# Kernel tuning notes

Measured on AMD Instinct MI355X. Metric: run time of the kernel, lower is better.

## Reference

```python
import jax, jax.numpy as jnp
import numpy as np

L = 6          # layers in stage
B = 8          # batch
NH = 16        # heads
F = 1024       # features per token
FH = F // NH   # features per head (64)
GH, GW = 24, 24
N = 1 + GH * GW  # 577 tokens (readout + patches)
HID = 4 * F


def _relpos_index():
    # BEiT-style relative position index over the (1+H*W) token grid
    coords = np.stack(np.meshgrid(np.arange(GH), np.arange(GW), indexing='ij')).reshape(2, -1)
    rel = (coords[:, :, None] - coords[:, None, :]).transpose(1, 2, 0).astype(np.int64)
    rel[..., 0] += GH - 1
    rel[..., 1] += GW - 1
    rel[..., 0] *= 2 * GW - 1
    nrd = (2 * GH - 1) * (2 * GW - 1) + 3  # num relative distances (+3 for readout token)
    idx = np.zeros((N, N), np.int64)
    idx[1:, 1:] = rel.sum(-1)
    idx[0, :] = nrd - 3
    idx[:, 0] = nrd - 2
    idx[0, 0] = nrd - 1
    return idx, nrd

REL_IDX_NP, NRD = _relpos_index()
REL_IDX = jnp.asarray(REL_IDX_NP)


def _ln(x, g, b):
    m = x.mean(-1, keepdims=True)
    v = ((x - m) ** 2).mean(-1, keepdims=True)
    return (x - m) / jnp.sqrt(v + 1e-6) * g + b


def setup_inputs() -> dict:
    key = jax.random.key(0)
    ks = jax.random.split(key, 16)
    s = 0.02
    return {
        'tokens': jax.random.normal(ks[0], (B, N, F), jnp.float32),
        'ln1_g': jnp.ones((L, F), jnp.float32),
        'ln1_b': jnp.zeros((L, F), jnp.float32),
        'q_bias': jax.random.normal(ks[1], (L, 1, NH, 1, FH), jnp.float32) * s,
        'v_bias': jax.random.normal(ks[2], (L, 1, NH, 1, FH), jnp.float32) * s,
        'qkv_w': jax.random.normal(ks[3], (L, 3 * F, F), jnp.float32) * s,
        'relpos_table': jax.random.normal(ks[4], (L, NRD, NH), jnp.float32) * s,
        'proj_w': jax.random.normal(ks[5], (L, F, F), jnp.float32) * s,
        'proj_b': jnp.zeros((L, F), jnp.float32),
        'scale_attn': jnp.full((L, F), 0.1, jnp.float32),
        'ln2_g': jnp.ones((L, F), jnp.float32),
        'ln2_b': jnp.zeros((L, F), jnp.float32),
        'mlp_w1': jax.random.normal(ks[6], (L, HID, F), jnp.float32) * s,
        'mlp_b1': jnp.zeros((L, HID), jnp.float32),
        'mlp_w2': jax.random.normal(ks[7], (L, F, HID), jnp.float32) * s,
        'mlp_b2': jnp.zeros((L, F), jnp.float32),
        'scale_mlp': jnp.full((L, F), 0.1, jnp.float32),
    }


def reference(tokens, ln1_g, ln1_b, q_bias, v_bias, qkv_w, relpos_table, proj_w, proj_b,
              scale_attn, ln2_g, ln2_b, mlp_w1, mlp_b1, mlp_w2, mlp_b2, scale_mlp):
    qk_scale = FH ** (-0.5)
    x = tokens
    for i in range(L):
        # --- attention branch ---
        h = _ln(x, ln1_g[i], ln1_b[i])                       # [B,N,F]
        qkv = (h @ qkv_w[i].T).reshape(B, N, 3, NH, FH)
        qkv = qkv.transpose(2, 0, 3, 1, 4)                   # [3,B,H,N,f]
        q = (qkv[0] + q_bias[i]) * qk_scale
        k = qkv[1]
        v = qkv[2] + v_bias[i]
        attn = jnp.einsum('bhnf,bhmf->bhnm', q, k)           # [B,H,N,N]
        bias = relpos_table[i][REL_IDX].transpose(2, 0, 1)   # [H,N,N]
        w = jax.nn.softmax(attn + bias[None], axis=-1)
        out = jnp.einsum('bhnm,bhmf->bhnf', w, v)
        out = out.transpose(0, 2, 1, 3).reshape(B, N, F)
        out = out @ proj_w[i].T + proj_b[i]
        x = x + scale_attn[i] * out
        # --- MLP branch ---
        h2 = _ln(x, ln2_g[i], ln2_b[i])
        m = jax.nn.gelu(h2 @ mlp_w1[i].T + mlp_b1[i], approximate=False)
        m = m @ mlp_w2[i].T + mlp_b2[i]
        x = x + scale_mlp[i] * m
    return x
```

## Files before the change

### kernel.cpp

```cpp
#include <hip/hip_runtime.h>
#include <cstdint>
#include <cstddef>

typedef __bf16 bf16;
typedef __bf16 bf16x8 __attribute__((ext_vector_type(8)));
typedef __bf16 bf16x4v __attribute__((ext_vector_type(4)));
typedef float f32x4 __attribute__((ext_vector_type(4)));
typedef unsigned int u32x4 __attribute__((ext_vector_type(4)));

static constexpr int NB = 8, NH = 16, F = 1024, FH = 64, NTOK = 577, NPAD = 640;
static constexpr int NLAYER = 6, HID = 4096, NRD = 2212;
static constexpr int MROWS = NB * NPAD;

static constexpr size_t H_OFF    = 0;
static constexpr size_t Q_OFF    = H_OFF    + (size_t)MROWS*F*2;
static constexpr size_t K_OFF    = Q_OFF    + (size_t)NB*NH*NPAD*FH*2;
static constexpr size_t V_OFF    = K_OFF    + (size_t)NB*NH*NPAD*FH*2;
static constexpr size_t O_OFF    = V_OFF    + (size_t)NB*NH*FH*NPAD*2;
static constexpr size_t BIAS_OFF = O_OFF    + (size_t)MROWS*F*2;
static constexpr size_t M1_OFF   = BIAS_OFF + (size_t)NH*NPAD*NPAD*4;
static constexpr size_t WQKV_OFF = M1_OFF   + (size_t)MROWS*HID*2;
static constexpr size_t WPROJ_OFF= WQKV_OFF + (size_t)3*F*F*2;
static constexpr size_t WM1_OFF  = WPROJ_OFF+ (size_t)F*F*2;
static constexpr size_t WM2_OFF  = WM1_OFF  + (size_t)HID*F*2;
static constexpr size_t WS_NEED  = WM2_OFF  + (size_t)HID*F*2;

__device__ __forceinline__ f32x4 mfma16(bf16x8 a, bf16x8 b, f32x4 c) {
  return __builtin_amdgcn_mfma_f32_16x16x32_bf16(a, b, c, 0, 0, 0);
}

__device__ __forceinline__ void gload16(const bf16* g, bf16* l) {
  __builtin_amdgcn_global_load_lds(
      (const __attribute__((address_space(1))) void*)g,
      (__attribute__((address_space(3))) void*)l, 16, 0, 0);
}

__global__ __launch_bounds__(256) void copy_kernel(const float* __restrict__ s, float* __restrict__ d) {
  size_t i = ((size_t)blockIdx.x*256 + threadIdx.x)*4;
  *(float4*)(d + i) = *(const float4*)(s + i);
}

static constexpr int CVT_N0 = 3*F*F;
static constexpr int CVT_N1 = CVT_N0 + F*F;
static constexpr int CVT_N2 = CVT_N1 + HID*F;
static constexpr int CVT_N3 = CVT_N2 + F*HID;
__global__ __launch_bounds__(256) void cvt4_kernel(
    const float* __restrict__ s0, const float* __restrict__ s1,
    const float* __restrict__ s2, const float* __restrict__ s3,
    bf16* __restrict__ d0, bf16* __restrict__ d1,
    bf16* __restrict__ d2, bf16* __restrict__ d3) {
  int i = (blockIdx.x*256 + threadIdx.x)*4;
  const float* s; bf16* d; int off;
  if (i < CVT_N0)      { s = s0; d = d0; off = i; }
  else if (i < CVT_N1) { s = s1; d = d1; off = i - CVT_N0; }
  else if (i < CVT_N2) { s = s2; d = d2; off = i - CVT_N1; }
  else                 { s = s3; d = d3; off = i - CVT_N2; }
  float4 v = *(const float4*)(s + off);
  bf16x4v o;
  o[0] = (bf16)v.x; o[1] = (bf16)v.y; o[2] = (bf16)v.z; o[3] = (bf16)v.w;
  *(bf16x4v*)(d + off) = o;
}

__global__ __launch_bounds__(256) void ln_kernel(const float* __restrict__ X,
    const float* __restrict__ g, const float* __restrict__ bta, bf16* __restrict__ H) {
  int row = blockIdx.x;
  int bb = row / NTOK, tok = row % NTOK;
  const float* x = X + (size_t)row * F;
  int tid = threadIdx.x;
  float4 v = *(const float4*)(x + tid*4);
  float s  = v.x + v.y + v.z + v.w;
  float s2 = v.x*v.x + v.y*v.y + v.z*v.z + v.w*v.w;
  #pragma unroll
  for (int off = 1; off < 64; off <<= 1) {
    s  += __shfl_xor(s,  off, 64);
    s2 += __shfl_xor(s2, off, 64);
  }
  __shared__ float red[8];
  int w = tid >> 6;
  if ((tid & 63) == 0) { red[w] = s; red[4+w] = s2; }
  __syncthreads();
  s  = red[0]+red[1]+red[2]+red[3];
  s2 = red[4]+red[5]+red[6]+red[7];
  float mean = s * (1.0f/1024.0f);
  float var  = s2 * (1.0f/1024.0f) - mean*mean;
  float rstd = rsqrtf(fmaxf(var, 0.0f) + 1e-6f);
  float4 gg  = *(const float4*)(g + tid*4);
  float4 bb4 = *(const float4*)(bta + tid*4);
  bf16x4v o;
  o[0] = (bf16)((v.x-mean)*rstd*gg.x + bb4.x);
  o[1] = (bf16)((v.y-mean)*rstd*gg.y + bb4.y);
  o[2] = (bf16)((v.z-mean)*rstd*gg.z + bb4.z);
  o[3] = (bf16)((v.w-mean)*rstd*gg.w + bb4.w);
  *(bf16x4v*)(H + ((size_t)bb*NPAD + tok)*F + tid*4) = o;
}

__global__ __launch_bounds__(256) void bias_kernel(const float* __restrict__ table, float* __restrict__ bias) {
  int bi = blockIdx.x;
  int h = bi / NPAD, n = bi % NPAD;
  float* out = bias + ((size_t)h*NPAD + n)*NPAD;
  for (int m = threadIdx.x; m < NPAD; m += 256) {
    float val;
    if (n >= NTOK || m >= NTOK) val = -1e30f;
    else {
      int idx;
      if (n == 0 && m == 0) idx = NRD - 1;
      else if (m == 0)      idx = NRD - 2;
      else if (n == 0)      idx = NRD - 3;
      else {
        int pn = n - 1, pm = m - 1;
        int rn = pn / 24, cn = pn % 24, rm = pm / 24, cm = pm % 24;
        idx = (rn - rm + 23)*47 + (cn - cm + 23);
      }
      val = table[idx*NH + h];
    }
    out[m] = val;
  }
}

template<int BMT, int EPI>
__global__ __launch_bounds__(256, 2)
void gemm_kernel(const bf16* __restrict__ A, const bf16* __restrict__ Bw, int K, int ldc,
                 const float* __restrict__ p0, const float* __restrict__ p1,
                 float* __restrict__ xout, bf16* __restrict__ bout,
                 bf16* __restrict__ q_out, bf16* __restrict__ k_out, bf16* __restrict__ v_out)
{
  constexpr int BM = 64*BMT;
  constexpr int WN = (BMT==2) ? 2 : 4;
  constexpr int NF = 128/(WN*16);
  __shared__ bf16 As[BM*32], Bs[128*32];
  const int tid = threadIdx.x;
  const int lane = tid & 63, w = tid >> 6;
  const int wm = (BMT==2) ? (w>>1) : 0;
  const int wn = (BMT==2) ? (w&1) : w;
  const int lg = lane >> 4, lr = lane & 15;
  const int m0 = blockIdx.x * BM, n0 = blockIdx.y * 128;

  const f32x4 fz = {0.f, 0.f, 0.f, 0.f};
  f32x4 acc[4][NF];
  #pragma unroll
  for (int i = 0; i < 4; ++i)
    #pragma unroll
    for (int j = 0; j < NF; ++j) acc[i][j] = fz;

  const int srow = lane >> 2;
  const int scol = (lane & 3) * 8;

  const int klen = K / (int)gridDim.z;
  const int kbeg = (int)blockIdx.z * klen;

  for (int kt = kbeg; kt < kbeg + klen; kt += 32) {
    if (BMT == 2) {
      #pragma unroll
      for (int j = 0; j < 2; ++j) {
        int li = w + j*4;
        gload16(A + (size_t)(m0 + li*16 + srow)*K + kt + scol, &As[li*512]);
      }
    } else {
      gload16(A + (size_t)(m0 + w*16 + srow)*K + kt + scol, &As[w*512]);
    }
    #pragma unroll
    for (int j = 0; j < 2; ++j) {
      int li = w*2 + j;
      gload16(Bw + (size_t)(n0 + li*16 + srow)*K + kt + scol, &Bs[li*512]);
    }
    __syncthreads();
    bf16x8 af[4], bfv[NF];
    #pragma unroll
    for (int f = 0; f < 4; ++f)
      af[f]  = *(const bf16x8*)&As[(wm*64 + f*16 + lr)*32 + lg*8];
    #pragma unroll
    for (int f = 0; f < NF; ++f)
      bfv[f] = *(const bf16x8*)&Bs[(wn*(NF*16) + f*16 + lr)*32 + lg*8];
    #pragma unroll
    for (int mf = 0; mf < 4; ++mf)
      #pragma unroll
      for (int nf = 0; nf < NF; ++nf)
        acc[mf][nf] = mfma16(af[mf], bfv[nf], acc[mf][nf]);
    __syncthreads();
  }

  #pragma unroll
  for (int mf = 0; mf < 4; ++mf) {
    const int row = m0 + wm*64 + mf*16 + lg*4;
    const int bidx = row / NPAD;
    const int tokbase = row - bidx*NPAD;
    #pragma unroll
    for (int nf = 0; nf < NF; ++nf) {
      const int col = n0 + wn*(NF*16) + nf*16 + lr;
      if (EPI == 0) {
        const int sec = col >> 10, ci = col & 1023;
        const int hh = ci >> 6, fh = ci & 63;
        const size_t bhh = (size_t)bidx*NH + hh;
        #pragma unroll
        for (int r = 0; r < 4; ++r) {
          float v = acc[mf][nf][r];
          if (sec == 0)      q_out[(bhh*NPAD + tokbase + r)*FH + fh] = (bf16)((v + p0[ci]) * 0.125f);
          else if (sec == 1) k_out[(bhh*NPAD + tokbase + r)*FH + fh] = (bf16)v;
          else               v_out[(bhh*FH + fh)*NPAD + tokbase + r] = (bf16)(v + p1[ci]);
        }
      } else if (EPI == 1) {
        const float pb = (blockIdx.z == 0) ? p0[col] : 0.0f;
        const float sc = p1[col];
        #pragma unroll
        for (int r = 0; r < 4; ++r) {
          int tok = tokbase + r;
          if (tok < NTOK) {
            size_t idx = ((size_t)bidx*NTOK + tok)*F + col;
            atomicAdd(xout + idx, sc * (acc[mf][nf][r] + pb));
          }
        }
      } else {
        const float pb = p0[col];
        #pragma unroll
        for (int r = 0; r < 4; ++r) {
          float t = acc[mf][nf][r] + pb;
          float gl = 0.5f*t*(1.0f + erff(t*0.70710678118f));
          bout[(size_t)(row + r)*ldc + col] = (bf16)gl;
        }
      }
    }
  }
}

__global__ __launch_bounds__(256, 2) void attn_kernel(
    const bf16* __restrict__ Qb, const bf16* __restrict__ Kb,
    const bf16* __restrict__ Vt, const float* __restrict__ Bias,
    bf16* __restrict__ O)
{
  __shared__ bf16 Qt[64*72], Kt[64*72], Vs[64*72], Pt[4][16*72];
  const int bh = blockIdx.x, rb = blockIdx.y;
  const int b = bh >> 4, h = bh & 15;
  const int tid = threadIdx.x, lane = tid & 63, w = tid >> 6;
  const int lg = lane >> 4, lr = lane & 15;

  const bf16*  Qg = Qb + ((size_t)bh*NPAD + rb*64)*FH;
  const bf16*  Kg = Kb + (size_t)bh*NPAD*FH;
  const bf16*  Vg = Vt + (size_t)bh*FH*NPAD;
  const float* Bg = Bias + (size_t)h*NPAD*NPAD;

  #pragma unroll
  for (int i = 0; i < 2; ++i) {
    int gidx = tid + i*256, r = gidx >> 3, cg = gidx & 7;
    *(u32x4*)&Qt[r*72 + cg*8] = *(const u32x4*)&Qg[r*64 + cg*8];
  }
  __syncthreads();
  bf16x8 qf0 = *(const bf16x8*)&Qt[(w*16+lr)*72 + lg*8];
  bf16x8 qf1 = *(const bf16x8*)&Qt[(w*16+lr)*72 + 32 + lg*8];

  const f32x4 fz = {0.f, 0.f, 0.f, 0.f};
  float m_run[4], l_run[4];
  f32x4 o_acc[4];
  #pragma unroll
  for (int r = 0; r < 4; ++r) { m_run[r] = -3.0e38f; l_run[r] = 0.0f; }
  #pragma unroll
  for (int f = 0; f < 4; ++f) o_acc[f] = fz;

  const int qrow = rb*64 + w*16 + lg*4;

  for (int cb = 0; cb < 10; ++cb) {
    __syncthreads();
    #pragma unroll
    for (int i = 0; i < 2; ++i) {
      int gidx = tid + i*256, r = gidx >> 3, cg = gidx & 7;
      *(u32x4*)&Kt[r*72 + cg*8] = *(const u32x4*)&Kg[(size_t)(cb*64+r)*64 + cg*8];
      *(u32x4*)&Vs[r*72 + cg*8] = *(const u32x4*)&Vg[(size_t)r*NPAD + cb*64 + cg*8];
    }
    __syncthreads();

    f32x4 s[4];
    #pragma unroll
    for (int nf = 0; nf < 4; ++nf) {
      bf16x8 k0 = *(const bf16x8*)&Kt[(nf*16+lr)*72 + lg*8];
      bf16x8 k1 = *(const bf16x8*)&Kt[(nf*16+lr)*72 + 32 + lg*8];
      s[nf] = mfma16(qf1, k1, mfma16(qf0, k0, fz));
    }
    #pragma unroll
    for (int nf = 0; nf < 4; ++nf)
      #pragma unroll
      for (int r = 0; r < 4; ++r)
        s[nf][r] += Bg[(size_t)(qrow + r)*NPAD + cb*64 + nf*16 + lr];

    float pm[4], sc[4], rs[4];
    #pragma unroll
    for (int r = 0; r < 4; ++r)
      pm[r] = fmaxf(fmaxf(s[0][r], s[1][r]), fmaxf(s[2][r], s[3][r]));
    #pragma unroll
    for (int off = 1; off < 16; off <<= 1)
      #pragma unroll
      for (int r = 0; r < 4; ++r)
        pm[r] = fmaxf(pm[r], __shfl_xor(pm[r], off, 64));
    #pragma unroll
    for (int r = 0; r < 4; ++r) {
      float mn = fmaxf(m_run[r], pm[r]);
      sc[r] = __expf(m_run[r] - mn);
      m_run[r] = mn;
      rs[r] = 0.0f;
    }
    #pragma unroll
    for (int nf = 0; nf < 4; ++nf)
      #pragma unroll
      for (int r = 0; r < 4; ++r) {
        float p = __expf(s[nf][r] - m_run[r]);
        s[nf][r] = p;
        rs[r] += p;
      }
    #pragma unroll
    for (int off = 1; off < 16; off <<= 1)
      #pragma unroll
      for (int r = 0; r < 4; ++r)
        rs[r] += __shfl_xor(rs[r], off, 64);
    #pragma unroll
    for (int r = 0; r < 4; ++r) l_run[r] = l_run[r]*sc[r] + rs[r];
    #pragma unroll
    for (int f = 0; f < 4; ++f) {
      o_acc[f][0] *= sc[0]; o_acc[f][1] *= sc[1];
      o_acc[f][2] *= sc[2]; o_acc[f][3] *= sc[3];
    }
    bf16* Ptw = &Pt[w][0];
    #pragma unroll
    for (int nf = 0; nf < 4; ++nf)
      #pragma unroll
      for (int r = 0; r < 4; ++r)
        Ptw[(lg*4 + r)*72 + nf*16 + lr] = (bf16)s[nf][r];
    __syncthreads();
    #pragma unroll
    for (int kc = 0; kc < 2; ++kc) {
      bf16x8 pa = *(const bf16x8*)&Ptw[lr*72 + kc*32 + lg*8];
      #pragma unroll
      for (int f = 0; f < 4; ++f) {
        bf16x8 vf = *(const bf16x8*)&Vs[(f*16+lr)*72 + kc*32 + lg*8];
        o_acc[f] = mfma16(pa, vf, o_acc[f]);
      }
    }
  }

  const int tokr = rb*64 + w*16 + lg*4;
  #pragma unroll
  for (int f = 0; f < 4; ++f)
    #pragma unroll
    for (int r = 0; r < 4; ++r) {
      float ov = o_acc[f][r] / l_run[r];
      O[((size_t)b*NPAD + tokr + r)*F + h*64 + f*16 + lr] = (bf16)ov;
    }
}

extern "C" void kernel_launch(void* const* d_in, const int* in_sizes, int n_in,
                              void* d_out, int out_size, void* d_ws, size_t ws_size,
                              hipStream_t stream) {
  (void)in_sizes; (void)n_in; (void)out_size;
  if (ws_size < WS_NEED) return;

  const float* tokens     = (const float*)d_in[0];
  const float* ln1_g      = (const float*)d_in[1];
  const float* ln1_b      = (const float*)d_in[2];
  const float* q_bias     = (const float*)d_in[3];
  const float* v_bias     = (const float*)d_in[4];
  const float* qkv_w      = (const float*)d_in[5];
  const float* relpos     = (const float*)d_in[6];
  const float* proj_w     = (const float*)d_in[7];
  const float* proj_b     = (const float*)d_in[8];
  const float* scale_attn = (const float*)d_in[9];
  const float* ln2_g      = (const float*)d_in[10];
  const float* ln2_b      = (const float*)d_in[11];
  const float* mlp_w1     = (const float*)d_in[12];
  const float* mlp_b1     = (const float*)d_in[13];
  const float* mlp_w2     = (const float*)d_in[14];
  const float* mlp_b2     = (const float*)d_in[15];
  const float* scale_mlp  = (const float*)d_in[16];

  char* ws = (char*)d_ws;
  bf16*  H     = (bf16*)(ws + H_OFF);
  bf16*  Qb    = (bf16*)(ws + Q_OFF);
  bf16*  Kb    = (bf16*)(ws + K_OFF);
  bf16*  Vt    = (bf16*)(ws + V_OFF);
  bf16*  Ob    = (bf16*)(ws + O_OFF);
  float* Bias  = (float*)(ws + BIAS_OFF);
  bf16*  M1    = (bf16*)(ws + M1_OFF);
  bf16*  Wqkv  = (bf16*)(ws + WQKV_OFF);
  bf16*  Wproj = (bf16*)(ws + WPROJ_OFF);
  bf16*  Wm1   = (bf16*)(ws + WM1_OFF);
  bf16*  Wm2   = (bf16*)(ws + WM2_OFF);
  float* X     = (float*)d_out;

  copy_kernel<<<NB*NTOK, 256, 0, stream>>>(tokens, X);

  for (int i = 0; i < NLAYER; ++i) {
    cvt4_kernel<<<CVT_N3/(256*4), 256, 0, stream>>>(
        qkv_w + (size_t)i*3*F*F, proj_w + (size_t)i*F*F,
        mlp_w1 + (size_t)i*HID*F, mlp_w2 + (size_t)i*F*HID,
        Wqkv, Wproj, Wm1, Wm2);
    bias_kernel<<<NH*NPAD, 256, 0, stream>>>(relpos + (size_t)i*NRD*NH, Bias);

    ln_kernel<<<NB*NTOK, 256, 0, stream>>>(X, ln1_g + i*F, ln1_b + i*F, H);
    gemm_kernel<2,0><<<dim3(MROWS/128, 3*F/128), 256, 0, stream>>>(
        H, Wqkv, F, 0, q_bias + i*F, v_bias + i*F,
        nullptr, nullptr, Qb, Kb, Vt);
    attn_kernel<<<dim3(NB*NH, NPAD/64), 256, 0, stream>>>(Qb, Kb, Vt, Bias, Ob);
    gemm_kernel<1,1><<<dim3(MROWS/64, F/128, 2), 256, 0, stream>>>(
        Ob, Wproj, F, 0, proj_b + i*F, scale_attn + i*F,
        X, nullptr, nullptr, nullptr, nullptr);

    ln_kernel<<<NB*NTOK, 256, 0, stream>>>(X, ln2_g + i*F, ln2_b + i*F, H);
    gemm_kernel<2,2><<<dim3(MROWS/128, HID/128), 256, 0, stream>>>(
        H, Wm1, F, HID, mlp_b1 + i*HID, nullptr,
        nullptr, M1, nullptr, nullptr, nullptr);
    gemm_kernel<1,1><<<dim3(MROWS/64, F/128, 2), 256, 0, stream>>>(
        M1, Wm2, HID, 0, mlp_b2 + i*F, scale_mlp + i*F,
        X, nullptr, nullptr, nullptr, nullptr);
  }
}
```

Measured before the change: 2.134 ms.

## Compute relative-position bias inside attention, drop proj split-K, retile MLP2 GEMM

Removes the separate bias_kernel and its 16x640x640 float bias tensor. The attention kernel now computes each relative-position index inline and gathers directly from the small relpos table, using multiply-shift division by 24. The projection GEMM no longer uses split-K: it launches with z=1 and does a plain read-modify-write instead of atomics. The MLP2 GEMM switches to 128-row tiles while keeping split-K of 2. This trades global bias-tensor traffic and one launch per layer for extra integer work and scattered table gathers in the attention inner loop, and halves the block count for the projection GEMM.

```diff
diff --git a/kernel.cpp b/kernel.cpp
--- a/kernel.cpp
+++ b/kernel.cpp
@@ -92,29 +92,6 @@
   o[2] = (bf16)((v.z-mean)*rstd*gg.z + bb4.z);
   o[3] = (bf16)((v.w-mean)*rstd*gg.w + bb4.w);
   *(bf16x4v*)(H + ((size_t)bb*NPAD + tok)*F + tid*4) = o;
-}
-
-__global__ __launch_bounds__(256) void bias_kernel(const float* __restrict__ table, float* __restrict__ bias) {
-  int bi = blockIdx.x;
-  int h = bi / NPAD, n = bi % NPAD;
-  float* out = bias + ((size_t)h*NPAD + n)*NPAD;
-  for (int m = threadIdx.x; m < NPAD; m += 256) {
-    float val;
-    if (n >= NTOK || m >= NTOK) val = -1e30f;
-    else {
-      int idx;
-      if (n == 0 && m == 0) idx = NRD - 1;
-      else if (m == 0)      idx = NRD - 2;
-      else if (n == 0)      idx = NRD - 3;
-      else {
-        int pn = n - 1, pm = m - 1;
-        int rn = pn / 24, cn = pn % 24, rm = pm / 24, cm = pm % 24;
-        idx = (rn - rm + 23)*47 + (cn - cm + 23);
-      }
-      val = table[idx*NH + h];
-    }
-    out[m] = val;
-  }
 }
 
 template<int BMT, int EPI>
@@ -206,7 +183,8 @@
           int tok = tokbase + r;
           if (tok < NTOK) {
             size_t idx = ((size_t)bidx*NTOK + tok)*F + col;
-            atomicAdd(xout + idx, sc * (acc[mf][nf][r] + pb));
+            if (gridDim.z == 1) xout[idx] += sc * (acc[mf][nf][r] + pb);
+            else                atomicAdd(xout + idx, sc * (acc[mf][nf][r] + pb));
           }
         }
       } else {
@@ -224,7 +202,7 @@
 
 __global__ __launch_bounds__(256, 2) void attn_kernel(
     const bf16* __restrict__ Qb, const bf16* __restrict__ Kb,
-    const bf16* __restrict__ Vt, const float* __restrict__ Bias,
+    const bf16* __restrict__ Vt, const float* __restrict__ Tg,
     bf16* __restrict__ O)
 {
   __shared__ bf16 Qt[64*72], Kt[64*72], Vs[64*72], Pt[4][16*72];
@@ -236,7 +214,6 @@
   const bf16*  Qg = Qb + ((size_t)bh*NPAD + rb*64)*FH;
   const bf16*  Kg = Kb + (size_t)bh*NPAD*FH;
   const bf16*  Vg = Vt + (size_t)bh*FH*NPAD;
-  const float* Bg = Bias + (size_t)h*NPAD*NPAD;
 
   #pragma unroll
   for (int i = 0; i < 2; ++i) {
@@ -256,6 +233,14 @@
   for (int f = 0; f < 4; ++f) o_acc[f] = fz;
 
   const int qrow = rb*64 + w*16 + lg*4;
+
+  int rnr[4], cnr[4];
+  #pragma unroll
+  for (int r = 0; r < 4; ++r) {
+    int pn = qrow + r - 1;
+    int rn = (pn * 2731) >> 16;
+    rnr[r] = rn; cnr[r] = pn - 24*rn;
+  }
 
   for (int cb = 0; cb < 10; ++cb) {
     __syncthreads();
@@ -275,23 +260,39 @@
       s[nf] = mfma16(qf1, k1, mfma16(qf0, k0, fz));
     }
     #pragma unroll
-    for (int nf = 0; nf < 4; ++nf)
+    for (int nf = 0; nf < 4; ++nf) {
+      const int m = cb*64 + nf*16 + lr;
+      const int pm = m - 1;
+      const int rm = (pm * 2731) >> 16;
+      const int cm = pm - 24*rm;
+      #pragma unroll
+      for (int r = 0; r < 4; ++r) {
+        const int n = qrow + r;
+        float bv;
+        if (n >= NTOK || m >= NTOK) bv = -1e30f;
+        else {
+          int idx;
+          if (m == 0)      idx = (n == 0) ? (NRD - 1) : (NRD - 2);
+          else if (n == 0) idx = NRD - 3;
+          else             idx = (rnr[r] - rm + 23)*47 + (cnr[r] - cm + 23);
+          bv = Tg[idx*NH + h];
+        }
+        s[nf][r] += bv;
+      }
+    }
+
+    float pm4[4], sc[4], rs[4];
+    #pragma unroll
+    for (int r = 0; r < 4; ++r)
+      pm4[r] = fmaxf(fmaxf(s[0][r], s[1][r]), fmaxf(s[2][r], s[3][r]));
+    #pragma unroll
+    for (int off = 1; off < 16; off <<= 1)
       #pragma unroll
       for (int r = 0; r < 4; ++r)
-        s[nf][r] += Bg[(size_t)(qrow + r)*NPAD + cb*64 + nf*16 + lr];
-
-    float pm[4], sc[4], rs[4];
-    #pragma unroll
-    for (int r = 0; r < 4; ++r)
-      pm[r] = fmaxf(fmaxf(s[0][r], s[1][r]), fmaxf(s[2][r], s[3][r]));
-    #pragma unroll
-    for (int off = 1; off < 16; off <<= 1)
-      #pragma unroll
-      for (int r = 0; r < 4; ++r)
-        pm[r] = fmaxf(pm[r], __shfl_xor(pm[r], off, 64));
+        pm4[r] = fmaxf(pm4[r], __shfl_xor(pm4[r], off, 64));
     #pragma unroll
     for (int r = 0; r < 4; ++r) {
-      float mn = fmaxf(m_run[r], pm[r]);
+      float mn = fmaxf(m_run[r], pm4[r]);
       sc[r] = __expf(m_run[r] - mn);
       m_run[r] = mn;
       rs[r] = 0.0f;
@@ -374,7 +375,6 @@
   bf16*  Kb    = (bf16*)(ws + K_OFF);
   bf16*  Vt    = (bf16*)(ws + V_OFF);
   bf16*  Ob    = (bf16*)(ws + O_OFF);
-  float* Bias  = (float*)(ws + BIAS_OFF);
   bf16*  M1    = (bf16*)(ws + M1_OFF);
   bf16*  Wqkv  = (bf16*)(ws + WQKV_OFF);
   bf16*  Wproj = (bf16*)(ws + WPROJ_OFF);
@@ -389,14 +389,14 @@
         qkv_w + (size_t)i*3*F*F, proj_w + (size_t)i*F*F,
         mlp_w1 + (size_t)i*HID*F, mlp_w2 + (size_t)i*F*HID,
         Wqkv, Wproj, Wm1, Wm2);
-    bias_kernel<<<NH*NPAD, 256, 0, stream>>>(relpos + (size_t)i*NRD*NH, Bias);
 
     ln_kernel<<<NB*NTOK, 256, 0, stream>>>(X, ln1_g + i*F, ln1_b + i*F, H);
     gemm_kernel<2,0><<<dim3(MROWS/128, 3*F/128), 256, 0, stream>>>(
         H, Wqkv, F, 0, q_bias + i*F, v_bias + i*F,
         nullptr, nullptr, Qb, Kb, Vt);
-    attn_kernel<<<dim3(NB*NH, NPAD/64), 256, 0, stream>>>(Qb, Kb, Vt, Bias, Ob);
-    gemm_kernel<1,1><<<dim3(MROWS/64, F/128, 2), 256, 0, stream>>>(
+    attn_kernel<<<dim3(NB*NH, NPAD/64), 256, 0, stream>>>(
+        Qb, Kb, Vt, relpos + (size_t)i*NRD*NH, Ob);
+    gemm_kernel<1,1><<<dim3(MROWS/64, F/128), 256, 0, stream>>>(
         Ob, Wproj, F, 0, proj_b + i*F, scale_attn + i*F,
         X, nullptr, nullptr, nullptr, nullptr);
 
@@ -404,7 +404,7 @@
     gemm_kernel<2,2><<<dim3(MROWS/128, HID/128), 256, 0, stream>>>(
         H, Wm1, F, HID, mlp_b1 + i*HID, nullptr,
         nullptr, M1, nullptr, nullptr, nullptr);
-    gemm_kernel<1,1><<<dim3(MROWS/64, F/128, 2), 256, 0, stream>>>(
+    gemm_kernel<2,1><<<dim3(MROWS/128, F/128, 2), 256, 0, stream>>>(
         M1, Wm2, HID, 0, mlp_b2 + i*F, scale_mlp + i*F,
         X, nullptr, nullptr, nullptr, nullptr);
   }
```

New measurement: 2.156 ms. Within noise of the previous version (+1.1%).
